# Kernel optimization log

Measured on AMD Instinct MI355X. Metric: run time of the kernel, lower is better.

## Reference

```python
import jax, jax.numpy as jnp
import numpy as np

K = 16
CIN = 128
COUT = 128
EPS = 1e-5
SLOPE = 0.01  # default negative_slope of nn.LeakyReLU


def _bn(w, gamma, beta):
    # BatchNorm1d in training mode over channel axis (last): stats over (N, k)
    mean = jnp.mean(w, axis=(0, 1))
    var = jnp.var(w, axis=(0, 1))  # biased variance, as torch uses for normalization
    return (w - mean) * jax.lax.rsqrt(var + EPS) * gamma + beta


def _leaky(x):
    return jnp.where(x >= 0, x, SLOPE * x)


def setup_inputs() -> dict:
    key = jax.random.key(0)
    ks = jax.random.split(key, 10)
    N = 8192
    s = 0.05
    return {
        "fea_i": jax.random.normal(ks[0], (N, CIN), jnp.float32),
        "fea_last": jax.random.normal(ks[1], (N, CIN), jnp.float32),
        "xyz_i": jax.random.uniform(ks[2], (N, 3), jnp.float32),
        "xyz_last": jax.random.uniform(ks[3], (N, 3), jnp.float32),
        "batch": jnp.zeros((N,), jnp.int32),
        "Wq": jax.random.normal(ks[4], (COUT, CIN), jnp.float32) * s,
        "bq": jnp.zeros((COUT,), jnp.float32),
        "Wk": jax.random.normal(ks[5], (COUT, CIN), jnp.float32) * s,
        "bk": jnp.zeros((COUT,), jnp.float32),
        "Wv": jax.random.normal(ks[6], (COUT, CIN), jnp.float32) * s,
        "bv": jnp.zeros((COUT,), jnp.float32),
        "bn1_gamma": jnp.ones((COUT,), jnp.float32),
        "bn1_beta": jnp.zeros((COUT,), jnp.float32),
        "Wl": jax.random.normal(ks[7], (COUT, COUT), jnp.float32) * s,
        "bl": jnp.zeros((COUT,), jnp.float32),
        "bn2_gamma": jnp.ones((COUT,), jnp.float32),
        "bn2_beta": jnp.zeros((COUT,), jnp.float32),
    }


def reference(fea_i, fea_last, xyz_i, xyz_last, batch, Wq, bq, Wk, bk, Wv, bv,
              bn1_gamma, bn1_beta, Wl, bl, bn2_gamma, bn2_beta):
    # knn: for each point in xyz_last, K nearest neighbors in xyz_i (single batch)
    d2 = jnp.sum((xyz_last[:, None, :] - xyz_i[None, :, :]) ** 2, axis=-1)  # (N, N)
    _, idx = jax.lax.top_k(-d2, K)  # (N, K) indices into xyz_i / fea_i

    fk = fea_i[idx]                                   # (N, K, CIN) gathered neighbor feats
    q = fea_last @ Wq.T + bq                          # (N, COUT); fea_last[idx_last] == row-repeat
    kk = jnp.einsum('nkc,oc->nko', fk, Wk) + bk       # (N, K, COUT)
    w = q[:, None, :] - kk                            # (N, K, COUT)

    # lin_w: BN -> LeakyReLU -> Linear -> BN -> LeakyReLU
    w = _leaky(_bn(w, bn1_gamma, bn1_beta))
    w = jnp.einsum('nko,po->nkp', w, Wl) + bl
    w = _leaky(_bn(w, bn2_gamma, bn2_beta))

    w = jax.nn.softmax(w, axis=1)                     # softmax over K neighbors
    v = jnp.einsum('nkc,oc->nko', fk, Wv) + bv        # (N, K, COUT)
    return jnp.sum(w * v, axis=1)                     # (N, COUT)
```

## Files before the change

### kernel.cpp

```cpp
#include <hip/hip_runtime.h>
#include <stdint.h>

#define NPTS   8192
#define NROWS  (NPTS * 16)
#define SLOPE  0.01f
#define BN_EPS 1e-5f

#define KNN_T2 0.04f
#define CAPQ   408
#define QPB    8
#define QPW    2

#define OFF_Q      0u
#define OFF_KP     4194304u
#define OFF_VP     8388608u
#define OFF_STATS  12582912u
#define OFF_XYZT   12845056u
#define OFF_IDX    13041664u
#define OFF_BIG    13585408u
#define WS_NEED    47139840u

typedef __bf16 bf16x8 __attribute__((ext_vector_type(8)));
typedef float  f32x4  __attribute__((ext_vector_type(4)));

__device__ __forceinline__ unsigned int pack_bf2(float lo, float hi) {
  unsigned int a = __float_as_uint(lo);
  unsigned int b = __float_as_uint(hi);
  unsigned int ra = (a + 0x7fffu + ((a >> 16) & 1u)) >> 16;
  unsigned int rb = (b + 0x7fffu + ((b >> 16) & 1u)) & 0xffff0000u;
  return ra | rb;
}
__device__ __forceinline__ unsigned short bf1(float v) {
  unsigned int a = __float_as_uint(v);
  return (unsigned short)((a + 0x7fffu + ((a >> 16) & 1u)) >> 16);
}
__device__ __forceinline__ float bf2f(unsigned short u) {
  return __uint_as_float(((unsigned int)u) << 16);
}

__device__ __forceinline__ void insert16(unsigned long long* key, unsigned long long kk) {
  if (kk < key[15]) {
    #pragma unroll
    for (int u = 15; u >= 1; --u) {
      bool cm1 = kk < key[u - 1];
      bool cs  = kk < key[u];
      key[u] = cm1 ? key[u - 1] : (cs ? kk : key[u]);
    }
    key[0] = (kk < key[0]) ? kk : key[0];
  }
}

__global__ __launch_bounds__(256) void k_prep(const float* __restrict__ xyz_i,
                                              const float* __restrict__ xyz_last,
                                              float* __restrict__ xyzT,
                                              float4* __restrict__ xyzp,
                                              float* __restrict__ stats_zero) {
  int t = blockIdx.x * 256 + threadIdx.x;
  {
    float x = xyz_i[t * 3 + 0], y = xyz_i[t * 3 + 1], z = xyz_i[t * 3 + 2];
    xyzp[t] = make_float4(x, y, z, fmaf(x, x, fmaf(y, y, z * z)));
    xyzT[3 * NPTS + t] = xyz_last[t * 3 + 0];
    xyzT[4 * NPTS + t] = xyz_last[t * 3 + 1];
    xyzT[5 * NPTS + t] = xyz_last[t * 3 + 2];
  }
  stats_zero[t] = 0.f;
}

__global__ __launch_bounds__(256) void k_proj(const float* __restrict__ fea_i,
                                              const float* __restrict__ fea_last,
                                              const float* __restrict__ Wq,
                                              const float* __restrict__ Wk,
                                              const float* __restrict__ Wv,
                                              const float* __restrict__ bq,
                                              const float* __restrict__ bk,
                                              const float* __restrict__ bv,
                                              float* __restrict__ Qo,
                                              float* __restrict__ Kpo,
                                              float* __restrict__ Vpo) {
  const int z = blockIdx.y;
  const float* A    = (z == 0) ? fea_last : fea_i;
  const float* W    = (z == 0) ? Wq : ((z == 1) ? Wk : Wv);
  const float* bias = (z == 0) ? bq : ((z == 1) ? bk : bv);
  float* Out        = (z == 0) ? Qo : ((z == 1) ? Kpo : Vpo);

  __shared__ unsigned short wl[128 * 128];
  const int t = threadIdx.x;
  const int lane = t & 63, w = t >> 6;

  #pragma unroll
  for (int i = 0; i < 8; ++i) {
    const int chunk = i * 256 + t;
    const int p = chunk >> 4, cseg = chunk & 15;
    const float4 wa = *(const float4*)(W + (size_t)p * 128 + cseg * 8);
    const float4 wb = *(const float4*)(W + (size_t)p * 128 + cseg * 8 + 4);
    uint4 pk;
    pk.x = pack_bf2(wa.x, wa.y); pk.y = pack_bf2(wa.z, wa.w);
    pk.z = pack_bf2(wb.x, wb.y); pk.w = pack_bf2(wb.z, wb.w);
    *(uint4*)((char*)wl + p * 256 + ((cseg * 16) ^ ((p & 7) << 4))) = pk;
  }
  __syncthreads();

  const int rowtile = blockIdx.x * 64 + w * 16;
  const int kslot = lane & 15, kgrp = lane >> 4;
  const float* Arow = A + (size_t)(rowtile + kslot) * 128;

  f32x4 acc[8];
  #pragma unroll
  for (int tt = 0; tt < 8; ++tt) acc[tt] = (f32x4){0.f, 0.f, 0.f, 0.f};

  #pragma unroll
  for (int s = 0; s < 4; ++s) {
    const int c0 = s * 32 + kgrp * 8;
    const float4 qa = *(const float4*)(Arow + c0);
    const float4 qb = *(const float4*)(Arow + c0 + 4);
    uint4 af;
    af.x = pack_bf2(qa.x, qa.y); af.y = pack_bf2(qa.z, qa.w);
    af.z = pack_bf2(qb.x, qb.y); af.w = pack_bf2(qb.z, qb.w);
    const bf16x8 Af = __builtin_bit_cast(bf16x8, af);
    const int cbyte = s * 64 + kgrp * 16;
    #pragma unroll
    for (int tt = 0; tt < 8; ++tt) {
      const int prow = tt * 16 + kslot;
      const uint4 bw = *(const uint4*)((const char*)wl + prow * 256 + (cbyte ^ ((prow & 7) << 4)));
      acc[tt] = __builtin_amdgcn_mfma_f32_16x16x32_bf16(Af, __builtin_bit_cast(bf16x8, bw), acc[tt], 0, 0, 0);
    }
  }

  #pragma unroll
  for (int tt = 0; tt < 8; ++tt) {
    const int col = tt * 16 + kslot;
    const float bb = bias[col];
    #pragma unroll
    for (int r = 0; r < 4; ++r) {
      const int row = rowtile + kgrp * 4 + r;
      Out[(size_t)row * 128 + col] = acc[tt][r] + bb;
    }
  }
}

__global__ __launch_bounds__(256) void k_knn(const float* __restrict__ xyzT,
                                             const float4* __restrict__ xyzp,
                                             const float* __restrict__ Q,
                                             const float* __restrict__ Kp,
                                             int* __restrict__ idxo,
                                             float* __restrict__ st1) {
  __shared__ float4 tile[512];
  __shared__ unsigned long long pool[QPB][CAPQ];
  __shared__ int sidx[4][QPW][16];
  __shared__ float red[4][256];
  const int t = threadIdx.x;
  const int lane = t & 63, wave = t >> 6;
  const int qq0 = wave * QPW;
  const int qbase = blockIdx.x * QPB + qq0;

  float qx[QPW], qy[QPW], qz[QPW];
  #pragma unroll
  for (int i = 0; i < QPW; ++i) {
    qx[i] = xyzT[3 * NPTS + qbase + i];
    qy[i] = xyzT[4 * NPTS + qbase + i];
    qz[i] = xyzT[5 * NPTS + qbase + i];
  }
  int cnt[QPW];
  #pragma unroll
  for (int i = 0; i < QPW; ++i) cnt[i] = 0;
  const unsigned long long below = (1ull << lane) - 1ull;

  float4 pf0 = xyzp[t], pf1 = xyzp[t + 256];
  for (int tb = 0; tb < 16; ++tb) {
    tile[t] = pf0; tile[t + 256] = pf1;
    __syncthreads();
    if (tb < 15) {
      pf0 = xyzp[(tb + 1) * 512 + t];
      pf1 = xyzp[(tb + 1) * 512 + t + 256];
    }
    const int pbase = tb * 512;
    #pragma unroll 2
    for (int it = 0; it < 8; ++it) {
      const float4 pp = tile[it * 64 + lane];
      const int p = pbase + it * 64 + lane;
      #pragma unroll
      for (int i = 0; i < QPW; ++i) {
        float dx = qx[i] - pp.x, dy = qy[i] - pp.y, dz = qz[i] - pp.z;
        float dd = fmaf(dx, dx, fmaf(dy, dy, dz * dz));
        bool g = dd < KNN_T2;
        unsigned long long mask = __ballot(g);
        int pos = cnt[i] + (int)__popcll(mask & below);
        if (g && pos < CAPQ)
          pool[qq0 + i][pos] = ((unsigned long long)__float_as_uint(dd) << 32) | (unsigned int)p;
        cnt[i] += (int)__popcll(mask);
      }
    }
    __syncthreads();
  }

  #pragma unroll 1
  for (int i = 0; i < QPW; ++i) {
    const int qq = qq0 + i;
    const int q = qbase + i;
    const int n = cnt[i];
    if (n >= 16 && n <= CAPQ) {
      unsigned long long lst[7];
      #pragma unroll
      for (int j = 0; j < 7; ++j) lst[j] = ~0ull;
      for (int j = lane; j < n; j += 64) {
        unsigned long long kk = pool[qq][j];
        #pragma unroll
        for (int u = 6; u >= 1; --u) {
          bool cm1 = kk < lst[u - 1];
          bool cs  = kk < lst[u];
          lst[u] = cm1 ? lst[u - 1] : (cs ? kk : lst[u]);
        }
        lst[0] = (kk < lst[0]) ? kk : lst[0];
      }
      int myidx = 0;
      #pragma unroll 1
      for (int r = 0; r < 16; ++r) {
        const float hd = __uint_as_float((unsigned int)(lst[0] >> 32));
        float wm = hd;
        #pragma unroll
        for (int o = 32; o; o >>= 1) wm = fminf(wm, __shfl_xor(wm, o));
        bool iswin = (hd == wm);
        const unsigned long long wmask = __ballot(iswin);
        unsigned int widx;
        if (__popcll(wmask) > 1) {
          unsigned int mi = iswin ? (unsigned int)lst[0] : 0xffffffffu;
          #pragma unroll
          for (int o = 32; o; o >>= 1) {
            unsigned int u = (unsigned int)__shfl_xor((int)mi, o);
            mi = (u < mi) ? u : mi;
          }
          widx = mi;
          iswin = iswin && ((unsigned int)lst[0] == mi);
        } else {
          const int wl = (int)__builtin_ctzll(wmask);
          widx = (unsigned int)__builtin_amdgcn_readlane((int)(unsigned int)lst[0], wl);
        }
        #pragma unroll
        for (int j = 0; j < 6; ++j) lst[j] = iswin ? lst[j + 1] : lst[j];
        lst[6] = iswin ? ~0ull : lst[6];
        if (lane == r) myidx = (int)widx;
      }
      if (lane < 16) {
        idxo[q * 16 + lane] = myidx;
        sidx[wave][i][lane] = myidx;
      }
    } else {
      unsigned long long key[16];
      #pragma unroll
      for (int j = 0; j < 16; ++j) key[j] = ~0ull;
      for (int it = 0; it < NPTS / 64; ++it) {
        const int p = it * 64 + lane;
        const float4 pp = xyzp[p];
        float dx = qx[i] - pp.x, dy = qy[i] - pp.y, dz = qz[i] - pp.z;
        float dd = fmaf(dx, dx, fmaf(dy, dy, dz * dz));
        insert16(key, ((unsigned long long)__float_as_uint(dd) << 32) | (unsigned int)p);
      }
      unsigned long long myout = ~0ull;
      #pragma unroll 1
      for (int r = 0; r < 16; ++r) {
        unsigned long long w = key[0];
        #pragma unroll
        for (int o = 32; o; o >>= 1) {
          unsigned long long u = __shfl_xor(w, o);
          w = (u < w) ? u : w;
        }
        if (key[0] == w) {
          #pragma unroll
          for (int j = 0; j < 15; ++j) key[j] = key[j + 1];
          key[15] = ~0ull;
        }
        if (lane == r) myout = w;
      }
      if (lane < 16) {
        idxo[q * 16 + lane] = (int)(myout & 0xffffffffull);
        sidx[wave][i][lane] = (int)(myout & 0xffffffffull);
      }
    }
  }

  const int c0 = lane * 2;
  float s0 = 0.f, s1 = 0.f, v0 = 0.f, v1 = 0.f;
  #pragma unroll
  for (int i = 0; i < QPW; ++i) {
    const int q = qbase + i;
    const float2 qv = *(const float2*)(Q + (size_t)q * 128 + c0);
    #pragma unroll 4
    for (int k = 0; k < 16; ++k) {
      const int pid = sidx[wave][i][k];
      const float2 kv = *(const float2*)(Kp + (size_t)pid * 128 + c0);
      const float w0 = qv.x - kv.x, w1 = qv.y - kv.y;
      s0 += w0; v0 += w0 * w0;
      s1 += w1; v1 += w1 * w1;
    }
  }
  red[wave][c0]       = s0;  red[wave][c0 + 1]       = s1;
  red[wave][128 + c0] = v0;  red[wave][129 + c0]     = v1;
  __syncthreads();
  {
    const float tot = red[0][t & 255] + red[1][t & 255] + red[2][t & 255] + red[3][t & 255];
    atomicAdd(&st1[(blockIdx.x & 15) * 256 + (t & 255)], tot);
  }
}

__global__ void k_bnfin(const float* __restrict__ stats, int nrep, float invM,
                        const float* __restrict__ gamma, const float* __restrict__ beta,
                        float* __restrict__ bn) {
  const int o = threadIdx.x;
  float s = 0.f, q = 0.f;
  for (int r = 0; r < nrep; ++r) { s += stats[r * 256 + o]; q += stats[r * 256 + 128 + o]; }
  float mean = s * invM;
  float var  = fmaf(-mean, mean, q * invM);
  float sc = gamma[o] * rsqrtf(var + BN_EPS);
  bn[o]       = sc;
  bn[128 + o] = fmaf(-mean, sc, beta[o]);
}

__global__ __launch_bounds__(256) void k_mid(const float* __restrict__ Q,
                                             const float* __restrict__ Kp,
                                             const int* __restrict__ idx,
                                             const float* __restrict__ Wl,
                                             const float* __restrict__ bl,
                                             const float* __restrict__ bn1,
                                             float* __restrict__ stats2,
                                             unsigned short* __restrict__ Y) {
  __shared__ union {
    unsigned short wl[128 * 128];
    struct {
      unsigned short stage[64][136];
      float red[4 * 256];
    } ep;
  } sm;

  const int t = threadIdx.x;
  const int lane = t & 63, w = t >> 6;
  const int rowbase = blockIdx.x * 64;

  #pragma unroll
  for (int i = 0; i < 8; ++i) {
    const int chunk = i * 256 + t;
    const int p = chunk >> 4, cseg = chunk & 15;
    const float4 wa = *(const float4*)(Wl + (size_t)p * 128 + cseg * 8);
    const float4 wb = *(const float4*)(Wl + (size_t)p * 128 + cseg * 8 + 4);
    uint4 pk;
    pk.x = pack_bf2(wa.x, wa.y); pk.y = pack_bf2(wa.z, wa.w);
    pk.z = pack_bf2(wb.x, wb.y); pk.w = pack_bf2(wb.z, wb.w);
    *(uint4*)((char*)sm.wl + p * 256 + ((cseg * 16) ^ ((p & 7) << 4))) = pk;
  }
  __syncthreads();

  const int n = blockIdx.x * 4 + w;
  const int kslot = lane & 15;
  const int kgrp  = lane >> 4;
  const int pid = idx[n * 16 + kslot];
  const float* Qrow = Q + (size_t)n * 128;
  const float* Krow = Kp + (size_t)pid * 128;

  f32x4 acc[8];
  #pragma unroll
  for (int tt = 0; tt < 8; ++tt) acc[tt] = (f32x4){0.f, 0.f, 0.f, 0.f};

  #pragma unroll
  for (int s = 0; s < 4; ++s) {
    const int c0 = s * 32 + kgrp * 8;
    const float4 qa = *(const float4*)(Qrow + c0);
    const float4 qb = *(const float4*)(Qrow + c0 + 4);
    const float4 ka = *(const float4*)(Krow + c0);
    const float4 kb = *(const float4*)(Krow + c0 + 4);
    const float4 sa = *(const float4*)(bn1 + c0);
    const float4 sb = *(const float4*)(bn1 + c0 + 4);
    const float4 ha = *(const float4*)(bn1 + 128 + c0);
    const float4 hb = *(const float4*)(bn1 + 128 + c0 + 4);
    float x[8];
    x[0] = fmaf(qa.x - ka.x, sa.x, ha.x);
    x[1] = fmaf(qa.y - ka.y, sa.y, ha.y);
    x[2] = fmaf(qa.z - ka.z, sa.z, ha.z);
    x[3] = fmaf(qa.w - ka.w, sa.w, ha.w);
    x[4] = fmaf(qb.x - kb.x, sb.x, hb.x);
    x[5] = fmaf(qb.y - kb.y, sb.y, hb.y);
    x[6] = fmaf(qb.z - kb.z, sb.z, hb.z);
    x[7] = fmaf(qb.w - kb.w, sb.w, hb.w);
    uint4 af;
    af.x = pack_bf2(fmaxf(x[0], SLOPE * x[0]), fmaxf(x[1], SLOPE * x[1]));
    af.y = pack_bf2(fmaxf(x[2], SLOPE * x[2]), fmaxf(x[3], SLOPE * x[3]));
    af.z = pack_bf2(fmaxf(x[4], SLOPE * x[4]), fmaxf(x[5], SLOPE * x[5]));
    af.w = pack_bf2(fmaxf(x[6], SLOPE * x[6]), fmaxf(x[7], SLOPE * x[7]));
    const bf16x8 A = __builtin_bit_cast(bf16x8, af);
    const int cbyte = s * 64 + kgrp * 16;
    #pragma unroll
    for (int tt = 0; tt < 8; ++tt) {
      const int prow = tt * 16 + kslot;
      const uint4 bw = *(const uint4*)((const char*)sm.wl + prow * 256 + (cbyte ^ ((prow & 7) << 4)));
      acc[tt] = __builtin_amdgcn_mfma_f32_16x16x32_bf16(A, __builtin_bit_cast(bf16x8, bw), acc[tt], 0, 0, 0);
    }
  }
  __syncthreads();

  #pragma unroll
  for (int tt = 0; tt < 8; ++tt) {
    const int col = tt * 16 + kslot;
    const float bb = bl[col];
    float s = 0.f, q2 = 0.f;
    #pragma unroll
    for (int r = 0; r < 4; ++r) {
      const float v = acc[tt][r] + bb;
      s += v; q2 += v * v;
      sm.ep.stage[w * 16 + kgrp * 4 + r][col] = bf1(v);
    }
    s  += __shfl_xor(s, 16);  s  += __shfl_xor(s, 32);
    q2 += __shfl_xor(q2, 16); q2 += __shfl_xor(q2, 32);
    if (kgrp == 0) {
      sm.ep.red[w * 256 + col]       = s;
      sm.ep.red[w * 256 + 128 + col] = q2;
    }
  }
  __syncthreads();

  #pragma unroll
  for (int i = 0; i < 4; ++i) {
    const int chunk = i * 256 + t;
    const int row = chunk >> 4, cc = chunk & 15;
    const uint4 v = *(const uint4*)&sm.ep.stage[row][cc * 8];
    *(uint4*)&Y[(size_t)(rowbase + row) * 128 + cc * 8] = v;
  }
  {
    const float tot = sm.ep.red[t] + sm.ep.red[256 + t] + sm.ep.red[512 + t] + sm.ep.red[768 + t];
    atomicAdd(&stats2[(blockIdx.x & 15) * 256 + t], tot);
  }
}

__global__ __launch_bounds__(128) void k_epi(const unsigned short* __restrict__ Y,
                                             const float* __restrict__ Vp,
                                             const int* __restrict__ idx,
                                             const float* __restrict__ bn2,
                                             float* __restrict__ out) {
  const int n = blockIdx.x;
  const int p = threadIdx.x;
  const float s2 = bn2[p], sh2 = bn2[128 + p];
  float z[16];
  #pragma unroll
  for (int k = 0; k < 16; ++k) {
    float yv = bf2f(Y[(size_t)(n * 16 + k) * 128 + p]);
    float v = fmaf(yv, s2, sh2);
    z[k] = (v >= 0.f) ? v : SLOPE * v;
  }
  float m = z[0];
  #pragma unroll
  for (int k = 1; k < 16; ++k) m = fmaxf(m, z[k]);
  float acc = 0.f, denom = 0.f;
  #pragma unroll
  for (int k = 0; k < 16; ++k) {
    float e = __expf(z[k] - m);
    denom += e;
    const int pid = idx[n * 16 + k];
    acc = fmaf(e, Vp[(size_t)pid * 128 + p], acc);
  }
  out[(size_t)n * 128 + p] = acc / denom;
}

extern "C" void kernel_launch(void* const* d_in, const int* in_sizes, int n_in,
                              void* d_out, int out_size, void* d_ws, size_t ws_size,
                              hipStream_t stream) {
  const float* fea_i    = (const float*)d_in[0];
  const float* fea_last = (const float*)d_in[1];
  const float* xyz_i    = (const float*)d_in[2];
  const float* xyz_last = (const float*)d_in[3];
  const float* Wq = (const float*)d_in[5];
  const float* bq = (const float*)d_in[6];
  const float* Wk = (const float*)d_in[7];
  const float* bk = (const float*)d_in[8];
  const float* Wv = (const float*)d_in[9];
  const float* bv = (const float*)d_in[10];
  const float* g1 = (const float*)d_in[11];
  const float* b1 = (const float*)d_in[12];
  const float* Wl = (const float*)d_in[13];
  const float* bl = (const float*)d_in[14];
  const float* g2 = (const float*)d_in[15];
  const float* b2 = (const float*)d_in[16];

  if (ws_size < (size_t)WS_NEED) return;

  char* ws = (char*)d_ws;
  float*  Q      = (float*)(ws + OFF_Q);
  float*  Kp     = (float*)(ws + OFF_KP);
  float*  Vp     = (float*)(ws + OFF_VP);
  float*  xyzT   = (float*)(ws + OFF_XYZT);
  int*    idxb   = (int*)  (ws + OFF_IDX);
  float*  st1    = (float*)(ws + OFF_STATS);
  float*  st2    = st1 + 4096;
  float*  bn1    = st1 + 8192;
  float*  bn2    = st1 + 8448;
  float4* xyzp   = (float4*)(ws + OFF_BIG);
  unsigned short* Y = (unsigned short*)(ws + OFF_BIG);

  k_prep<<<32, 256, 0, stream>>>(xyz_i, xyz_last, xyzT, xyzp, st1);
  k_proj<<<dim3(128, 3), 256, 0, stream>>>(fea_i, fea_last, Wq, Wk, Wv, bq, bk, bv, Q, Kp, Vp);
  k_knn<<<NPTS / QPB, 256, 0, stream>>>(xyzT, xyzp, Q, Kp, idxb, st1);
  k_bnfin<<<1, 128, 0, stream>>>(st1, 16, 1.f / (float)NROWS, g1, b1, bn1);
  k_mid<<<2048, 256, 0, stream>>>(Q, Kp, idxb, Wl, bl, bn1, st2, Y);
  k_bnfin<<<1, 128, 0, stream>>>(st2, 16, 1.f / (float)NROWS, g2, b2, bn2);
  k_epi<<<8192, 128, 0, stream>>>(Y, Vp, idxb, bn2, (float*)d_out);
}
```

Before: 125.6 us.

## Replace brute-force KNN scan with uniform grid binning and radius-limited cell search

Builds an 8x8x8 uniform grid over xyz_i using count, prefix-sum and scatter kernels, then each wave scans only the cells overlapping a small ball around its query point, falling back to a larger radius and finally to a full scan. This removes the all-pairs distance pass over all 8192 points per query. In exchange it adds three small serial kernels with atomics and uses divergent per-row loops. BN partial sums are now added with per-wave atomics instead of a block reduction in shared memory.

```diff
diff --git a/kernel.cpp b/kernel.cpp
--- a/kernel.cpp
+++ b/kernel.cpp
@@ -6,19 +6,26 @@
 #define SLOPE  0.01f
 #define BN_EPS 1e-5f
 
-#define KNN_T2 0.04f
-#define CAPQ   408
-#define QPB    8
-#define QPW    2
+#define TP     0.13f
+#define TP2    (TP * TP)
+#define CAP    152
+#define TF     0.2f
+#define TF2    0.04f
+#define CAPF   408
+#define EPSB   1e-5f
 
 #define OFF_Q      0u
 #define OFF_KP     4194304u
 #define OFF_VP     8388608u
 #define OFF_STATS  12582912u
-#define OFF_XYZT   12845056u
+#define OFF_TAB    12845056u
 #define OFF_IDX    13041664u
 #define OFF_BIG    13585408u
 #define WS_NEED    47139840u
+
+#define T_PCNT 0
+#define T_POFF 512
+#define T_PCUR 1025
 
 typedef __bf16 bf16x8 __attribute__((ext_vector_type(8)));
 typedef float  f32x4  __attribute__((ext_vector_type(4)));
@@ -38,6 +45,13 @@
   return __uint_as_float(((unsigned int)u) << 16);
 }
 
+__device__ __forceinline__ int cell_of(float x, float y, float z) {
+  int cx = min(7, max(0, (int)(x * 8.f)));
+  int cy = min(7, max(0, (int)(y * 8.f)));
+  int cz = min(7, max(0, (int)(z * 8.f)));
+  return (cz * 8 + cy) * 8 + cx;
+}
+
 __device__ __forceinline__ void insert16(unsigned long long* key, unsigned long long kk) {
   if (kk < key[15]) {
     #pragma unroll
@@ -50,20 +64,132 @@
   }
 }
 
-__global__ __launch_bounds__(256) void k_prep(const float* __restrict__ xyz_i,
-                                              const float* __restrict__ xyz_last,
-                                              float* __restrict__ xyzT,
-                                              float4* __restrict__ xyzp,
-                                              float* __restrict__ stats_zero) {
-  int t = blockIdx.x * 256 + threadIdx.x;
-  {
-    float x = xyz_i[t * 3 + 0], y = xyz_i[t * 3 + 1], z = xyz_i[t * 3 + 2];
-    xyzp[t] = make_float4(x, y, z, fmaf(x, x, fmaf(y, y, z * z)));
-    xyzT[3 * NPTS + t] = xyz_last[t * 3 + 0];
-    xyzT[4 * NPTS + t] = xyz_last[t * 3 + 1];
-    xyzT[5 * NPTS + t] = xyz_last[t * 3 + 2];
-  }
-  stats_zero[t] = 0.f;
+template<int D>
+__device__ __forceinline__ void extract_topk(const unsigned long long* __restrict__ poolq, int n, int lane,
+                                             int* __restrict__ sidxq, int* __restrict__ idxoq) {
+  unsigned long long lst[D];
+  #pragma unroll
+  for (int j = 0; j < D; ++j) lst[j] = ~0ull;
+  for (int j = lane; j < n; j += 64) {
+    unsigned long long kk = poolq[j];
+    #pragma unroll
+    for (int u = D - 1; u >= 1; --u) {
+      bool cm1 = kk < lst[u - 1];
+      bool cs  = kk < lst[u];
+      lst[u] = cm1 ? lst[u - 1] : (cs ? kk : lst[u]);
+    }
+    lst[0] = (kk < lst[0]) ? kk : lst[0];
+  }
+  int myidx = 0;
+  #pragma unroll 1
+  for (int r = 0; r < 16; ++r) {
+    const float hd = __uint_as_float((unsigned int)(lst[0] >> 32));
+    float wm = hd;
+    #pragma unroll
+    for (int o = 32; o; o >>= 1) wm = fminf(wm, __shfl_xor(wm, o));
+    bool iswin = (hd == wm);
+    const unsigned long long wmask = __ballot(iswin);
+    unsigned int widx;
+    if (__popcll(wmask) > 1) {
+      unsigned int mi = iswin ? (unsigned int)lst[0] : 0xffffffffu;
+      #pragma unroll
+      for (int o = 32; o; o >>= 1) {
+        unsigned int u = (unsigned int)__shfl_xor((int)mi, o);
+        mi = (u < mi) ? u : mi;
+      }
+      widx = mi;
+      iswin = iswin && ((unsigned int)lst[0] == mi);
+    } else {
+      const int wl = (int)__builtin_ctzll(wmask);
+      widx = (unsigned int)__builtin_amdgcn_readlane((int)(unsigned int)lst[0], wl);
+    }
+    #pragma unroll
+    for (int u = 0; u < D - 1; ++u) lst[u] = iswin ? lst[u + 1] : lst[u];
+    lst[D - 1] = iswin ? ~0ull : lst[D - 1];
+    if (lane == r) myidx = (int)widx;
+  }
+  if (lane < 16) { idxoq[lane] = myidx; sidxq[lane] = myidx; }
+}
+
+__device__ __forceinline__ int scan_ball(const int* __restrict__ poff, const float4* __restrict__ bp,
+                                         float qx, float qy, float qz, float rad, float r2, int cap,
+                                         unsigned long long* __restrict__ poolw,
+                                         int lane, unsigned long long below) {
+  const int lx = max(0, (int)floorf((qx - rad - EPSB) * 8.f));
+  const int hx = min(7, (int)floorf((qx + rad + EPSB) * 8.f));
+  const int ly = max(0, (int)floorf((qy - rad - EPSB) * 8.f));
+  const int hy = min(7, (int)floorf((qy + rad + EPSB) * 8.f));
+  const int lz = max(0, (int)floorf((qz - rad - EPSB) * 8.f));
+  const int hz = min(7, (int)floorf((qz + rad + EPSB) * 8.f));
+  const int nrY = hy - ly + 1, nrows = nrY * (hz - lz + 1);
+  int zi = 0;
+  #pragma unroll
+  for (int z2 = 1; z2 < 5; ++z2) zi += (lane >= z2 * nrY) ? 1 : 0;
+  const int yi = lane - zi * nrY;
+  int rs = 0, re = 0;
+  if (lane < nrows) {
+    const int crow = ((lz + zi) * 8 + (ly + yi)) * 8;
+    rs = poff[crow + lx]; re = poff[crow + hx + 1];
+  }
+  int cnt = 0;
+  for (int r = 0; r < nrows; ++r) {
+    const int rsr = __builtin_amdgcn_readlane(rs, r);
+    const int rer = __builtin_amdgcn_readlane(re, r);
+    for (int base = rsr; base < rer; base += 64) {
+      const int pos = base + lane;
+      const float4 pp = bp[pos];
+      float dx = qx - pp.x, dy = qy - pp.y, dz = qz - pp.z;
+      float dd = fmaf(dx, dx, fmaf(dy, dy, dz * dz));
+      bool g = (pos < rer) && (dd < r2);
+      unsigned long long mask = __ballot(g);
+      int p2 = cnt + (int)__popcll(mask & below);
+      if (g && p2 < cap)
+        poolw[p2] = ((unsigned long long)__float_as_uint(dd) << 32) | (unsigned int)__float_as_int(pp.w);
+      cnt += (int)__popcll(mask);
+    }
+  }
+  return cnt;
+}
+
+__global__ __launch_bounds__(256) void k_zero(int* __restrict__ tab,
+                                              float* __restrict__ stats,
+                                              float4* __restrict__ bp) {
+  const int T = blockIdx.x * 256 + threadIdx.x;
+  if (T < 8192) stats[T] = 0.f;
+  if (T < 512)  tab[T_PCNT + T] = 0;
+  if (T < 64)   bp[NPTS + T] = make_float4(1e9f, 1e9f, 1e9f, __int_as_float(0));
+}
+
+__global__ __launch_bounds__(256) void k_count(const float* __restrict__ xyz_i,
+                                               int* __restrict__ tab) {
+  const int t = blockIdx.x * 256 + threadIdx.x;
+  atomicAdd(&tab[T_PCNT + cell_of(xyz_i[t * 3], xyz_i[t * 3 + 1], xyz_i[t * 3 + 2])], 1);
+}
+
+__global__ __launch_bounds__(512) void k_offsets(int* __restrict__ tab) {
+  __shared__ int ls[512];
+  const int t = threadIdx.x;
+  const int v = tab[T_PCNT + t];
+  ls[t] = v;
+  __syncthreads();
+  for (int ofs = 1; ofs < 512; ofs <<= 1) {
+    int add = (t >= ofs) ? ls[t - ofs] : 0;
+    __syncthreads();
+    ls[t] += add;
+    __syncthreads();
+  }
+  tab[T_POFF + t] = ls[t] - v;
+  tab[T_PCUR + t] = ls[t] - v;
+  if (t == 511) tab[T_POFF + 512] = ls[511];
+}
+
+__global__ __launch_bounds__(256) void k_scatter(const float* __restrict__ xyz_i,
+                                                 int* __restrict__ tab,
+                                                 float4* __restrict__ bp) {
+  const int t = blockIdx.x * 256 + threadIdx.x;
+  float x = xyz_i[t * 3], y = xyz_i[t * 3 + 1], z = xyz_i[t * 3 + 2];
+  int pos = atomicAdd(&tab[T_PCUR + cell_of(x, y, z)], 1);
+  bp[pos] = make_float4(x, y, z, __int_as_float(t));
 }
 
 __global__ __launch_bounds__(256) void k_proj(const float* __restrict__ fea_i,
@@ -138,122 +264,39 @@
   }
 }
 
-__global__ __launch_bounds__(256) void k_knn(const float* __restrict__ xyzT,
-                                             const float4* __restrict__ xyzp,
+__global__ __launch_bounds__(256) void k_knn(const int* __restrict__ tab,
+                                             const float4* __restrict__ bp,
+                                             const float* __restrict__ xyz_last,
                                              const float* __restrict__ Q,
                                              const float* __restrict__ Kp,
                                              int* __restrict__ idxo,
                                              float* __restrict__ st1) {
-  __shared__ float4 tile[512];
-  __shared__ unsigned long long pool[QPB][CAPQ];
-  __shared__ int sidx[4][QPW][16];
-  __shared__ float red[4][256];
-  const int t = threadIdx.x;
-  const int lane = t & 63, wave = t >> 6;
-  const int qq0 = wave * QPW;
-  const int qbase = blockIdx.x * QPB + qq0;
-
-  float qx[QPW], qy[QPW], qz[QPW];
-  #pragma unroll
-  for (int i = 0; i < QPW; ++i) {
-    qx[i] = xyzT[3 * NPTS + qbase + i];
-    qy[i] = xyzT[4 * NPTS + qbase + i];
-    qz[i] = xyzT[5 * NPTS + qbase + i];
-  }
-  int cnt[QPW];
-  #pragma unroll
-  for (int i = 0; i < QPW; ++i) cnt[i] = 0;
+  __shared__ unsigned long long pool[4][CAPF];
+  __shared__ int sidx[4][16];
+  const int t = threadIdx.x, lane = t & 63, wave = t >> 6;
+  const int q = blockIdx.x * 4 + wave;
+  const float qx = xyz_last[q * 3];
+  const float qy = xyz_last[q * 3 + 1];
+  const float qz = xyz_last[q * 3 + 2];
+  const int* poff = &tab[T_POFF];
   const unsigned long long below = (1ull << lane) - 1ull;
 
-  float4 pf0 = xyzp[t], pf1 = xyzp[t + 256];
-  for (int tb = 0; tb < 16; ++tb) {
-    tile[t] = pf0; tile[t + 256] = pf1;
-    __syncthreads();
-    if (tb < 15) {
-      pf0 = xyzp[(tb + 1) * 512 + t];
-      pf1 = xyzp[(tb + 1) * 512 + t + 256];
-    }
-    const int pbase = tb * 512;
-    #pragma unroll 2
-    for (int it = 0; it < 8; ++it) {
-      const float4 pp = tile[it * 64 + lane];
-      const int p = pbase + it * 64 + lane;
-      #pragma unroll
-      for (int i = 0; i < QPW; ++i) {
-        float dx = qx[i] - pp.x, dy = qy[i] - pp.y, dz = qz[i] - pp.z;
-        float dd = fmaf(dx, dx, fmaf(dy, dy, dz * dz));
-        bool g = dd < KNN_T2;
-        unsigned long long mask = __ballot(g);
-        int pos = cnt[i] + (int)__popcll(mask & below);
-        if (g && pos < CAPQ)
-          pool[qq0 + i][pos] = ((unsigned long long)__float_as_uint(dd) << 32) | (unsigned int)p;
-        cnt[i] += (int)__popcll(mask);
-      }
-    }
-    __syncthreads();
-  }
-
-  #pragma unroll 1
-  for (int i = 0; i < QPW; ++i) {
-    const int qq = qq0 + i;
-    const int q = qbase + i;
-    const int n = cnt[i];
-    if (n >= 16 && n <= CAPQ) {
-      unsigned long long lst[7];
-      #pragma unroll
-      for (int j = 0; j < 7; ++j) lst[j] = ~0ull;
-      for (int j = lane; j < n; j += 64) {
-        unsigned long long kk = pool[qq][j];
-        #pragma unroll
-        for (int u = 6; u >= 1; --u) {
-          bool cm1 = kk < lst[u - 1];
-          bool cs  = kk < lst[u];
-          lst[u] = cm1 ? lst[u - 1] : (cs ? kk : lst[u]);
-        }
-        lst[0] = (kk < lst[0]) ? kk : lst[0];
-      }
-      int myidx = 0;
-      #pragma unroll 1
-      for (int r = 0; r < 16; ++r) {
-        const float hd = __uint_as_float((unsigned int)(lst[0] >> 32));
-        float wm = hd;
-        #pragma unroll
-        for (int o = 32; o; o >>= 1) wm = fminf(wm, __shfl_xor(wm, o));
-        bool iswin = (hd == wm);
-        const unsigned long long wmask = __ballot(iswin);
-        unsigned int widx;
-        if (__popcll(wmask) > 1) {
-          unsigned int mi = iswin ? (unsigned int)lst[0] : 0xffffffffu;
-          #pragma unroll
-          for (int o = 32; o; o >>= 1) {
-            unsigned int u = (unsigned int)__shfl_xor((int)mi, o);
-            mi = (u < mi) ? u : mi;
-          }
-          widx = mi;
-          iswin = iswin && ((unsigned int)lst[0] == mi);
-        } else {
-          const int wl = (int)__builtin_ctzll(wmask);
-          widx = (unsigned int)__builtin_amdgcn_readlane((int)(unsigned int)lst[0], wl);
-        }
-        #pragma unroll
-        for (int j = 0; j < 6; ++j) lst[j] = iswin ? lst[j + 1] : lst[j];
-        lst[6] = iswin ? ~0ull : lst[6];
-        if (lane == r) myidx = (int)widx;
-      }
-      if (lane < 16) {
-        idxo[q * 16 + lane] = myidx;
-        sidx[wave][i][lane] = myidx;
-      }
+  int cnt = scan_ball(poff, bp, qx, qy, qz, TP, TP2, CAP, &pool[wave][0], lane, below);
+  if (cnt >= 16 && cnt <= CAP) {
+    extract_topk<3>(&pool[wave][0], cnt, lane, &sidx[wave][0], &idxo[q * 16]);
+  } else {
+    cnt = scan_ball(poff, bp, qx, qy, qz, TF, TF2, CAPF, &pool[wave][0], lane, below);
+    if (cnt >= 16 && cnt <= CAPF) {
+      extract_topk<7>(&pool[wave][0], cnt, lane, &sidx[wave][0], &idxo[q * 16]);
     } else {
       unsigned long long key[16];
       #pragma unroll
-      for (int j = 0; j < 16; ++j) key[j] = ~0ull;
+      for (int u = 0; u < 16; ++u) key[u] = ~0ull;
       for (int it = 0; it < NPTS / 64; ++it) {
-        const int p = it * 64 + lane;
-        const float4 pp = xyzp[p];
-        float dx = qx[i] - pp.x, dy = qy[i] - pp.y, dz = qz[i] - pp.z;
+        const float4 pp = bp[it * 64 + lane];
+        float dx = qx - pp.x, dy = qy - pp.y, dz = qz - pp.z;
         float dd = fmaf(dx, dx, fmaf(dy, dy, dz * dz));
-        insert16(key, ((unsigned long long)__float_as_uint(dd) << 32) | (unsigned int)p);
+        insert16(key, ((unsigned long long)__float_as_uint(dd) << 32) | (unsigned int)__float_as_int(pp.w));
       }
       unsigned long long myout = ~0ull;
       #pragma unroll 1
@@ -266,40 +309,34 @@
         }
         if (key[0] == w) {
           #pragma unroll
-          for (int j = 0; j < 15; ++j) key[j] = key[j + 1];
+          for (int u = 0; u < 15; ++u) key[u] = key[u + 1];
           key[15] = ~0ull;
         }
         if (lane == r) myout = w;
       }
       if (lane < 16) {
         idxo[q * 16 + lane] = (int)(myout & 0xffffffffull);
-        sidx[wave][i][lane] = (int)(myout & 0xffffffffull);
+        sidx[wave][lane] = (int)(myout & 0xffffffffull);
       }
     }
   }
 
   const int c0 = lane * 2;
+  const float2 qv = *(const float2*)(Q + (size_t)q * 128 + c0);
   float s0 = 0.f, s1 = 0.f, v0 = 0.f, v1 = 0.f;
-  #pragma unroll
-  for (int i = 0; i < QPW; ++i) {
-    const int q = qbase + i;
-    const float2 qv = *(const float2*)(Q + (size_t)q * 128 + c0);
-    #pragma unroll 4
-    for (int k = 0; k < 16; ++k) {
-      const int pid = sidx[wave][i][k];
-      const float2 kv = *(const float2*)(Kp + (size_t)pid * 128 + c0);
-      const float w0 = qv.x - kv.x, w1 = qv.y - kv.y;
-      s0 += w0; v0 += w0 * w0;
-      s1 += w1; v1 += w1 * w1;
-    }
-  }
-  red[wave][c0]       = s0;  red[wave][c0 + 1]       = s1;
-  red[wave][128 + c0] = v0;  red[wave][129 + c0]     = v1;
-  __syncthreads();
-  {
-    const float tot = red[0][t & 255] + red[1][t & 255] + red[2][t & 255] + red[3][t & 255];
-    atomicAdd(&st1[(blockIdx.x & 15) * 256 + (t & 255)], tot);
-  }
+  #pragma unroll 4
+  for (int k = 0; k < 16; ++k) {
+    const int pid = sidx[wave][k];
+    const float2 kv = *(const float2*)(Kp + (size_t)pid * 128 + c0);
+    const float w0 = qv.x - kv.x, w1 = qv.y - kv.y;
+    s0 += w0; v0 += w0 * w0;
+    s1 += w1; v1 += w1 * w1;
+  }
+  const int slot = (blockIdx.x & 15) * 256;
+  atomicAdd(&st1[slot + c0],       s0);
+  atomicAdd(&st1[slot + c0 + 1],   s1);
+  atomicAdd(&st1[slot + 128 + c0], v0);
+  atomicAdd(&st1[slot + 129 + c0], v1);
 }
 
 __global__ void k_bnfin(const float* __restrict__ stats, int nrep, float invM,
@@ -483,18 +520,21 @@
   float*  Q      = (float*)(ws + OFF_Q);
   float*  Kp     = (float*)(ws + OFF_KP);
   float*  Vp     = (float*)(ws + OFF_VP);
-  float*  xyzT   = (float*)(ws + OFF_XYZT);
+  int*    tab    = (int*)  (ws + OFF_TAB);
   int*    idxb   = (int*)  (ws + OFF_IDX);
   float*  st1    = (float*)(ws + OFF_STATS);
   float*  st2    = st1 + 4096;
   float*  bn1    = st1 + 8192;
   float*  bn2    = st1 + 8448;
-  float4* xyzp   = (float4*)(ws + OFF_BIG);
+  float4* bp     = (float4*)(ws + OFF_BIG);
   unsigned short* Y = (unsigned short*)(ws + OFF_BIG);
 
-  k_prep<<<32, 256, 0, stream>>>(xyz_i, xyz_last, xyzT, xyzp, st1);
+  k_zero<<<33, 256, 0, stream>>>(tab, st1, bp);
   k_proj<<<dim3(128, 3), 256, 0, stream>>>(fea_i, fea_last, Wq, Wk, Wv, bq, bk, bv, Q, Kp, Vp);
-  k_knn<<<NPTS / QPB, 256, 0, stream>>>(xyzT, xyzp, Q, Kp, idxb, st1);
+  k_count<<<32, 256, 0, stream>>>(xyz_i, tab);
+  k_offsets<<<1, 512, 0, stream>>>(tab);
+  k_scatter<<<32, 256, 0, stream>>>(xyz_i, tab, bp);
+  k_knn<<<2048, 256, 0, stream>>>(tab, bp, xyz_last, Q, Kp, idxb, st1);
   k_bnfin<<<1, 128, 0, stream>>>(st1, 16, 1.f / (float)NROWS, g1, b1, bn1);
   k_mid<<<2048, 256, 0, stream>>>(Q, Kp, idxb, Wl, bl, bn1, st2, Y);
   k_bnfin<<<1, 128, 0, stream>>>(st2, 16, 1.f / (float)NROWS, g2, b2, bn2);
```

New measurement: 126.5 us. Within noise of the previous version (+0.8%).
